# Optimization experiments

Measured on AMD Instinct MI355X. Metric: run time of the kernel, lower is better.

The kernel has to match this reference:

```python
import jax, jax.numpy as jnp
import numpy as np

B, T, F, H, E = 512, 512, 32, 128, 64


def _uniform(key, shape, fan):
    bound = 1.0 / np.sqrt(fan)
    return jax.random.uniform(key, shape, jnp.float32, -bound, bound)


def setup_inputs() -> dict:
    key = jax.random.key(0)
    ks = jax.random.split(key, 9)
    return {
        "x": jax.random.normal(ks[0], (B, T, F), jnp.float32),
        # layer 1: n_features -> hidden_dim (PyTorch gate order i,f,g,o)
        "W_ih1": _uniform(ks[1], (4 * H, F), H),
        "W_hh1": _uniform(ks[2], (4 * H, H), H),
        "b_ih1": _uniform(ks[3], (4 * H,), H),
        "b_hh1": _uniform(ks[4], (4 * H,), H),
        # layer 2: hidden_dim -> embedding_dim
        "W_ih2": _uniform(ks[5], (4 * E, H), E),
        "W_hh2": _uniform(ks[6], (4 * E, E), E),
        "b_ih2": _uniform(ks[7], (4 * E,), E),
        "b_hh2": _uniform(ks[8], (4 * E,), E),
    }


def _lstm(x_seq, W_ih, W_hh, b_ih, b_hh):
    """batch_first LSTM, zero init state. Returns (all_h [B,T,H], last_h [B,H])."""
    b, t, _ = x_seq.shape
    h_dim = W_hh.shape[1]
    # precompute input contributions for the whole sequence: [B,T,4H]
    xg = jnp.einsum('bti,gi->btg', x_seq, W_ih) + b_ih + b_hh

    def step(carry, xt):
        h, c = carry
        gates = xt + h @ W_hh.T  # [B,4H]
        i, f, g, o = jnp.split(gates, 4, axis=-1)
        i = jax.nn.sigmoid(i)
        f = jax.nn.sigmoid(f)
        g = jnp.tanh(g)
        o = jax.nn.sigmoid(o)
        c = f * c + i * g
        h = o * jnp.tanh(c)
        return (h, c), h

    h0 = jnp.zeros((b, h_dim), x_seq.dtype)
    (hT, _), hs = jax.lax.scan(step, (h0, h0), jnp.swapaxes(xg, 0, 1))
    return jnp.swapaxes(hs, 0, 1), hT


def reference(x, W_ih1, W_hh1, b_ih1, b_hh1, W_ih2, W_hh2, b_ih2, b_hh2):
    x = x.reshape((-1, T, F))
    seq1, _ = _lstm(x, W_ih1, W_hh1, b_ih1, b_hh1)       # [B,T,H]
    _, hT = _lstm(seq1, W_ih2, W_hh2, b_ih2, b_hh2)       # [B,E]
    return hT
```

## Files before the change

kernel.cpp:

```cpp
#include <hip/hip_runtime.h>

typedef __attribute__((ext_vector_type(8))) _Float16 halfx8;
typedef __attribute__((ext_vector_type(4))) float f32x4;

#define MFMA16H(a, b, c) __builtin_amdgcn_mfma_f32_16x16x32_f16(a, b, c, 0, 0, 0)

#define T_SEQ 512
#define F_IN 32
#define H1 128
#define E2 64
#define ROWS 4

__device__ __forceinline__ ushort f2h(float f) {
    _Float16 h = (_Float16)f;
    return __builtin_bit_cast(ushort, h);
}
__device__ __forceinline__ float fast_sigmoid(float x) {
    float e = __expf(-x);
    return __builtin_amdgcn_rcpf(1.0f + e);
}
__device__ __forceinline__ float fast_tanh(float x) {
    float e = __expf(-2.0f * x);
    return 2.0f * __builtin_amdgcn_rcpf(1.0f + e) - 1.0f;
}
__device__ __forceinline__ halfx8 load_w8h(const float* p) {
    halfx8 r;
#pragma unroll
    for (int j = 0; j < 8; ++j) r[j] = (_Float16)p[j];
    return r;
}

__global__ __launch_bounds__(512, 1) void lstm_fused(
    const float* __restrict__ x,
    const float* __restrict__ Wih1,
    const float* __restrict__ Whh1,
    const float* __restrict__ bih1,
    const float* __restrict__ bhh1,
    const float* __restrict__ Wih2,
    const float* __restrict__ Whh2,
    const float* __restrict__ bih2,
    const float* __restrict__ bhh2,
    float* __restrict__ out)
{
    __shared__ __align__(16) ushort xs [16][ROWS][80];
    __shared__ __align__(16) ushort h1s[2][ROWS][144];
    __shared__ __align__(16) ushort h2s[2][ROWS][80];

    const int tid  = threadIdx.x;
    const int wave = tid >> 6;
    const int lane = tid & 63;
    const int l15  = lane & 15;
    const int quad = lane >> 4;
    const int arow = l15 >> 2;
    const int r0   = blockIdx.x * ROWS;
    const bool isL1 = (wave < 4);
    const int w    = wave & 3;

    halfx8 wf[40];
    float  bias[8];

    if (isL1) {
#pragma unroll
        for (int g = 0; g < 4; ++g)
#pragma unroll
            for (int uo = 0; uo < 2; ++uo) {
                const int tau = g * 2 + uo;
                const int n = g * 128 + w * 32 + uo * 16 + l15;
#pragma unroll
                for (int kt = 0; kt < 4; ++kt)
                    wf[tau * 4 + kt] = load_w8h(Whh1 + n * H1 + kt * 32 + quad * 8);
                wf[32 + tau] = load_w8h(Wih1 + n * F_IN + quad * 8);
                bias[tau] = bih1[n] + bhh1[n];
            }
    } else {
#pragma unroll
        for (int g = 0; g < 4; ++g) {
            const int n = g * 64 + w * 16 + l15;
#pragma unroll
            for (int kt = 0; kt < 4; ++kt)
                wf[g * 4 + kt] = load_w8h(Wih2 + n * H1 + kt * 32 + quad * 8);
#pragma unroll
            for (int kc = 0; kc < 2; ++kc)
                wf[16 + g * 2 + kc] = load_w8h(Whh2 + n * E2 + kc * 32 + quad * 8);
            bias[g] = bih2[n] + bhh2[n];
        }
    }

    for (int i = tid; i < 2 * ROWS * 144; i += 512) ((ushort*)h1s)[i] = 0;
    for (int i = tid; i < 2 * ROWS * 80;  i += 512) ((ushort*)h2s)[i] = 0;

    float cst[2] = {0.0f, 0.0f};

    const int xrow = w;
    const int xcol = lane;
    const bool stager = (!isL1) && (lane < 32);
    const float* xptr = x + ((size_t)(r0 + xrow) * T_SEQ) * F_IN + xcol;
    float xr8[8];
#pragma unroll
    for (int j = 0; j < 8; ++j) xr8[j] = 0.0f;
    if (stager) {
        float t0[8];
#pragma unroll
        for (int j = 0; j < 8; ++j) t0[j] = xptr[(size_t)j * F_IN];
#pragma unroll
        for (int j = 0; j < 8; ++j) xs[j][xrow][xcol] = f2h(t0[j]);
#pragma unroll
        for (int j = 0; j < 8; ++j) xr8[j] = xptr[(size_t)(8 + j) * F_IN];
    }
    __syncthreads();

    f32x4 acc[8];

#pragma unroll 1
    for (int tt = 0; tt <= T_SEQ; ++tt) {
        const int p  = tt & 1;
        const int pn = p ^ 1;

        if (isL1) {
            if (tt < T_SEQ) {
#pragma unroll
                for (int tau = 0; tau < 8; ++tau)
                    acc[tau] = (f32x4){bias[tau], bias[tau], bias[tau], bias[tau]};
                __builtin_amdgcn_s_setprio(1);
                {
                    const halfx8 ax = *(const halfx8*)&xs[tt & 15][arow][quad * 8];
#pragma unroll
                    for (int tau = 0; tau < 8; ++tau)
                        acc[tau] = MFMA16H(ax, wf[32 + tau], acc[tau]);
                }
#pragma unroll
                for (int kt = 0; kt < 4; ++kt) {
                    const halfx8 a = *(const halfx8*)&h1s[p][arow][kt * 32 + quad * 8];
#pragma unroll
                    for (int tau = 0; tau < 8; ++tau)
                        acc[tau] = MFMA16H(a, wf[tau * 4 + kt], acc[tau]);
                }
                __builtin_amdgcn_s_setprio(0);
#pragma unroll
                for (int uo = 0; uo < 2; ++uo) {
                    const int u = w * 32 + uo * 16 + l15;
                    const float iv = fast_sigmoid(acc[0 + uo][0]);
                    const float fv = fast_sigmoid(acc[2 + uo][0]);
                    const float gv = fast_tanh   (acc[4 + uo][0]);
                    const float ov = fast_sigmoid(acc[6 + uo][0]);
                    const float cn = fv * cst[uo] + iv * gv;
                    cst[uo] = cn;
                    const float h = ov * fast_tanh(cn);
                    h1s[pn][quad][u] = f2h(h);
                }
            }
        } else {
            if (tt >= 1) {
#pragma unroll
                for (int g = 0; g < 4; ++g)
                    acc[g] = (f32x4){bias[g], bias[g], bias[g], bias[g]};
                __builtin_amdgcn_s_setprio(1);
#pragma unroll
                for (int kt = 0; kt < 4; ++kt) {
                    const halfx8 a = *(const halfx8*)&h1s[p][arow][kt * 32 + quad * 8];
#pragma unroll
                    for (int g = 0; g < 4; ++g)
                        acc[g] = MFMA16H(a, wf[g * 4 + kt], acc[g]);
                }
#pragma unroll
                for (int kc = 0; kc < 2; ++kc) {
                    const halfx8 a = *(const halfx8*)&h2s[p][arow][kc * 32 + quad * 8];
#pragma unroll
                    for (int g = 0; g < 4; ++g)
                        acc[g] = MFMA16H(a, wf[16 + g * 2 + kc], acc[g]);
                }
                __builtin_amdgcn_s_setprio(0);
                const int u = w * 16 + l15;
                const float iv = fast_sigmoid(acc[0][0]);
                const float fv = fast_sigmoid(acc[1][0]);
                const float gv = fast_tanh   (acc[2][0]);
                const float ov = fast_sigmoid(acc[3][0]);
                const float cn = fv * cst[0] + iv * gv;
                cst[0] = cn;
                const float h = ov * fast_tanh(cn);
                if (tt == T_SEQ) {
                    out[(size_t)(r0 + quad) * E2 + u] = h;
                } else {
                    h2s[pn][quad][u] = f2h(h);
                }
            }
            if (stager && (tt & 7) == 0) {
#pragma unroll
                for (int j = 0; j < 8; ++j) {
                    const int t = tt + 8 + j;
                    if (t < T_SEQ) xs[t & 15][xrow][xcol] = f2h(xr8[j]);
                }
#pragma unroll
                for (int j = 0; j < 8; ++j) {
                    const int t = tt + 16 + j;
                    if (t < T_SEQ) xr8[j] = xptr[(size_t)t * F_IN];
                }
            }
        }
        __syncthreads();
    }
}

extern "C" void kernel_launch(void* const* d_in, const int* in_sizes, int n_in,
                              void* d_out, int out_size, void* d_ws, size_t ws_size,
                              hipStream_t stream) {
    lstm_fused<<<128, 512, 0, stream>>>(
        (const float*)d_in[0], (const float*)d_in[1], (const float*)d_in[2],
        (const float*)d_in[3], (const float*)d_in[4], (const float*)d_in[5],
        (const float*)d_in[6], (const float*)d_in[7], (const float*)d_in[8],
        (float*)d_out);
}
```

Measured before the change: 475.4 us.

## Offload layer-1 input projection to layer-2 waves, batched four timesteps ahead

The layer-1 input projection (x·W_ih1 + bias) moves off the critical layer-1 recurrence. The layer-2 waves now compute it every 4 steps, one MFMA per gate tile covering 4 timesteps × 4 rows, and write it into an 8-slot LDS ring. The layer-1 waves then run only the recurrent h·W_hh1 MFMAs and add the precomputed gate inputs. The aim is to shorten the serial per-step chain on the layer-1 waves. The cost is extra LDS traffic, extra register pressure on the layer-2 waves, and relying on the ring's slot timing staying correct.

```diff
diff --git a/kernel.cpp b/kernel.cpp
--- a/kernel.cpp
+++ b/kernel.cpp
@@ -42,9 +42,11 @@
     const float* __restrict__ bhh2,
     float* __restrict__ out)
 {
-    __shared__ __align__(16) ushort xs [16][ROWS][80];
+    __shared__ __align__(16) ushort xa [4][16][40];
+    __shared__ __align__(16) float  xgl[8 * 2088];
     __shared__ __align__(16) ushort h1s[2][ROWS][144];
     __shared__ __align__(16) ushort h2s[2][ROWS][80];
+#define XGI(s, r, u) ((s) * 2088 + (r) * 520 + (u) * 4)
 
     const int tid  = threadIdx.x;
     const int wave = tid >> 6;
@@ -56,8 +58,8 @@
     const bool isL1 = (wave < 4);
     const int w    = wave & 3;
 
-    halfx8 wf[40];
-    float  bias[8];
+    halfx8 wf[32];
+    float  bias2[4], bx[8];
 
     if (isL1) {
 #pragma unroll
@@ -69,21 +71,28 @@
 #pragma unroll
                 for (int kt = 0; kt < 4; ++kt)
                     wf[tau * 4 + kt] = load_w8h(Whh1 + n * H1 + kt * 32 + quad * 8);
-                wf[32 + tau] = load_w8h(Wih1 + n * F_IN + quad * 8);
-                bias[tau] = bih1[n] + bhh1[n];
             }
     } else {
 #pragma unroll
         for (int g = 0; g < 4; ++g) {
-            const int n = g * 64 + w * 16 + l15;
+            const int n2 = g * 64 + w * 16 + l15;
 #pragma unroll
             for (int kt = 0; kt < 4; ++kt)
-                wf[g * 4 + kt] = load_w8h(Wih2 + n * H1 + kt * 32 + quad * 8);
+                wf[g * 4 + kt] = load_w8h(Wih2 + n2 * H1 + kt * 32 + quad * 8);
 #pragma unroll
             for (int kc = 0; kc < 2; ++kc)
-                wf[16 + g * 2 + kc] = load_w8h(Whh2 + n * E2 + kc * 32 + quad * 8);
-            bias[g] = bih2[n] + bhh2[n];
+                wf[16 + g * 2 + kc] = load_w8h(Whh2 + n2 * E2 + kc * 32 + quad * 8);
+            bias2[g] = bih2[n2] + bhh2[n2];
         }
+#pragma unroll
+        for (int g = 0; g < 4; ++g)
+#pragma unroll
+            for (int uo = 0; uo < 2; ++uo) {
+                const int tau = g * 2 + uo;
+                const int n = g * 128 + w * 32 + uo * 16 + l15;
+                wf[24 + tau] = load_w8h(Wih1 + n * F_IN + quad * 8);
+                bx[tau] = bih1[n] + bhh1[n];
+            }
     }
 
     for (int i = tid; i < 2 * ROWS * 144; i += 512) ((ushort*)h1s)[i] = 0;
@@ -91,10 +100,8 @@
 
     float cst[2] = {0.0f, 0.0f};
 
-    const int xrow = w;
-    const int xcol = lane;
     const bool stager = (!isL1) && (lane < 32);
-    const float* xptr = x + ((size_t)(r0 + xrow) * T_SEQ) * F_IN + xcol;
+    const float* xptr = x + ((size_t)(r0 + w) * T_SEQ) * F_IN + lane;
     float xr8[8];
 #pragma unroll
     for (int j = 0; j < 8; ++j) xr8[j] = 0.0f;
@@ -103,13 +110,27 @@
 #pragma unroll
         for (int j = 0; j < 8; ++j) t0[j] = xptr[(size_t)j * F_IN];
 #pragma unroll
-        for (int j = 0; j < 8; ++j) xs[j][xrow][xcol] = f2h(t0[j]);
+        for (int j = 0; j < 8; ++j)
+            xa[(j >> 2) & 3][(j & 3) * 4 + w][lane] = f2h(t0[j]);
 #pragma unroll
         for (int j = 0; j < 8; ++j) xr8[j] = xptr[(size_t)(8 + j) * F_IN];
     }
     __syncthreads();
 
-    f32x4 acc[8];
+    if (!isL1) {
+        const halfx8 af = *(const halfx8*)&xa[0][l15][quad * 8];
+#pragma unroll
+        for (int nt = 0; nt < 8; ++nt) {
+            const float b = bx[nt];
+            const f32x4 cinit = {b, b, b, b};
+            const f32x4 d = MFMA16H(af, wf[24 + nt], cinit);
+            const int uu = w * 32 + (nt & 1) * 16 + l15;
+#pragma unroll
+            for (int j = 0; j < 4; ++j)
+                xgl[XGI(quad, j, uu) + (nt >> 1)] = d[j];
+        }
+    }
+    __syncthreads();
 
 #pragma unroll 1
     for (int tt = 0; tt <= T_SEQ; ++tt) {
@@ -118,31 +139,31 @@
 
         if (isL1) {
             if (tt < T_SEQ) {
+                const f32x4 xg0 = *(const f32x4*)&xgl[XGI(tt & 7, quad, w * 32 + l15)];
+                const f32x4 xg1 = *(const f32x4*)&xgl[XGI(tt & 7, quad, w * 32 + 16 + l15)];
+                halfx8 hf[4];
+#pragma unroll
+                for (int kt = 0; kt < 4; ++kt)
+                    hf[kt] = *(const halfx8*)&h1s[p][arow][kt * 32 + quad * 8];
+                f32x4 acc[8];
 #pragma unroll
                 for (int tau = 0; tau < 8; ++tau)
-                    acc[tau] = (f32x4){bias[tau], bias[tau], bias[tau], bias[tau]};
+                    acc[tau] = (f32x4){0.0f, 0.0f, 0.0f, 0.0f};
                 __builtin_amdgcn_s_setprio(1);
-                {
-                    const halfx8 ax = *(const halfx8*)&xs[tt & 15][arow][quad * 8];
+#pragma unroll
+                for (int kt = 0; kt < 4; ++kt)
 #pragma unroll
                     for (int tau = 0; tau < 8; ++tau)
-                        acc[tau] = MFMA16H(ax, wf[32 + tau], acc[tau]);
-                }
-#pragma unroll
-                for (int kt = 0; kt < 4; ++kt) {
-                    const halfx8 a = *(const halfx8*)&h1s[p][arow][kt * 32 + quad * 8];
-#pragma unroll
-                    for (int tau = 0; tau < 8; ++tau)
-                        acc[tau] = MFMA16H(a, wf[tau * 4 + kt], acc[tau]);
-                }
+                        acc[tau] = MFMA16H(hf[kt], wf[tau * 4 + kt], acc[tau]);
                 __builtin_amdgcn_s_setprio(0);
 #pragma unroll
                 for (int uo = 0; uo < 2; ++uo) {
+                    const f32x4 xgv = uo ? xg1 : xg0;
                     const int u = w * 32 + uo * 16 + l15;
-                    const float iv = fast_sigmoid(acc[0 + uo][0]);
-                    const float fv = fast_sigmoid(acc[2 + uo][0]);
-                    const float gv = fast_tanh   (acc[4 + uo][0]);
-                    const float ov = fast_sigmoid(acc[6 + uo][0]);
+                    const float iv = fast_sigmoid(acc[0 + uo][0] + xgv[0]);
+                    const float fv = fast_sigmoid(acc[2 + uo][0] + xgv[1]);
+                    const float gv = fast_tanh   (acc[4 + uo][0] + xgv[2]);
+                    const float ov = fast_sigmoid(acc[6 + uo][0] + xgv[3]);
                     const float cn = fv * cst[uo] + iv * gv;
                     cst[uo] = cn;
                     const float h = ov * fast_tanh(cn);
@@ -151,30 +172,31 @@
             }
         } else {
             if (tt >= 1) {
+                f32x4 acc2[4];
 #pragma unroll
                 for (int g = 0; g < 4; ++g)
-                    acc[g] = (f32x4){bias[g], bias[g], bias[g], bias[g]};
+                    acc2[g] = (f32x4){bias2[g], bias2[g], bias2[g], bias2[g]};
                 __builtin_amdgcn_s_setprio(1);
 #pragma unroll
                 for (int kt = 0; kt < 4; ++kt) {
                     const halfx8 a = *(const halfx8*)&h1s[p][arow][kt * 32 + quad * 8];
 #pragma unroll
                     for (int g = 0; g < 4; ++g)
-                        acc[g] = MFMA16H(a, wf[g * 4 + kt], acc[g]);
+                        acc2[g] = MFMA16H(a, wf[g * 4 + kt], acc2[g]);
                 }
 #pragma unroll
                 for (int kc = 0; kc < 2; ++kc) {
                     const halfx8 a = *(const halfx8*)&h2s[p][arow][kc * 32 + quad * 8];
 #pragma unroll
                     for (int g = 0; g < 4; ++g)
-                        acc[g] = MFMA16H(a, wf[16 + g * 2 + kc], acc[g]);
+                        acc2[g] = MFMA16H(a, wf[16 + g * 2 + kc], acc2[g]);
                 }
                 __builtin_amdgcn_s_setprio(0);
                 const int u = w * 16 + l15;
-                const float iv = fast_sigmoid(acc[0][0]);
-                const float fv = fast_sigmoid(acc[1][0]);
-                const float gv = fast_tanh   (acc[2][0]);
-                const float ov = fast_sigmoid(acc[3][0]);
+                const float iv = fast_sigmoid(acc2[0][0]);
+                const float fv = fast_sigmoid(acc2[1][0]);
+                const float gv = fast_tanh   (acc2[2][0]);
+                const float ov = fast_sigmoid(acc2[3][0]);
                 const float cn = fv * cst[0] + iv * gv;
                 cst[0] = cn;
                 const float h = ov * fast_tanh(cn);
@@ -184,11 +206,29 @@
                     h2s[pn][quad][u] = f2h(h);
                 }
             }
+            if ((tt & 3) == 0) {
+                const int tb = (tt >> 2) + 1;
+                if (tb < (T_SEQ >> 2)) {
+                    const halfx8 af = *(const halfx8*)&xa[tb & 3][l15][quad * 8];
+#pragma unroll
+                    for (int nt = 0; nt < 8; ++nt) {
+                        const float b = bx[nt];
+                        const f32x4 cinit = {b, b, b, b};
+                        const f32x4 d = MFMA16H(af, wf[24 + nt], cinit);
+                        const int uu = w * 32 + (nt & 1) * 16 + l15;
+                        const int slot = (tb * 4 + quad) & 7;
+#pragma unroll
+                        for (int j = 0; j < 4; ++j)
+                            xgl[XGI(slot, j, uu) + (nt >> 1)] = d[j];
+                    }
+                }
+            }
             if (stager && (tt & 7) == 0) {
 #pragma unroll
                 for (int j = 0; j < 8; ++j) {
                     const int t = tt + 8 + j;
-                    if (t < T_SEQ) xs[t & 15][xrow][xcol] = f2h(xr8[j]);
+                    if (t < T_SEQ)
+                        xa[(t >> 2) & 3][(t & 3) * 4 + w][lane] = f2h(xr8[j]);
                 }
 #pragma unroll
                 for (int j = 0; j < 8; ++j) {
@@ -199,6 +239,7 @@
         }
         __syncthreads();
     }
+#undef XGI
 }
 
 extern "C" void kernel_launch(void* const* d_in, const int* in_sizes, int n_in,
```

Result: slower. 516.1 us (+8.6%).

## Split layer-1 LSTM work across eight waves with 768-thread blocks

Applied to the files above, without the earlier changes.

Layer 1 now runs on 8 waves instead of 4, each owning 16 hidden units (4 gate tiles) instead of 32, which halves the serial MFMA chain per wave on the critical recurrent step. Blocks grow to 768 threads, and layer-2 waves become waves 8-11. The h1 LDS fragments are also loaded up front, before the MFMA chain starts. The cost is more waves per CU taking part in each per-step barrier, plus more threads contending for the single CU's issue slots.

```diff
diff --git a/kernel.cpp b/kernel.cpp
--- a/kernel.cpp
+++ b/kernel.cpp
@@ -30,7 +30,7 @@
     return r;
 }
 
-__global__ __launch_bounds__(512, 1) void lstm_fused(
+__global__ __launch_bounds__(768, 1) void lstm_fused(
     const float* __restrict__ x,
     const float* __restrict__ Wih1,
     const float* __restrict__ Whh1,
@@ -53,29 +53,26 @@
     const int quad = lane >> 4;
     const int arow = l15 >> 2;
     const int r0   = blockIdx.x * ROWS;
-    const bool isL1 = (wave < 4);
-    const int w    = wave & 3;
-
-    halfx8 wf[40];
-    float  bias[8];
+    const bool isL1 = (wave < 8);
+
+    halfx8 wf[24];
+    float  bias[4];
 
     if (isL1) {
 #pragma unroll
-        for (int g = 0; g < 4; ++g)
-#pragma unroll
-            for (int uo = 0; uo < 2; ++uo) {
-                const int tau = g * 2 + uo;
-                const int n = g * 128 + w * 32 + uo * 16 + l15;
-#pragma unroll
-                for (int kt = 0; kt < 4; ++kt)
-                    wf[tau * 4 + kt] = load_w8h(Whh1 + n * H1 + kt * 32 + quad * 8);
-                wf[32 + tau] = load_w8h(Wih1 + n * F_IN + quad * 8);
-                bias[tau] = bih1[n] + bhh1[n];
-            }
+        for (int g = 0; g < 4; ++g) {
+            const int n = g * 128 + wave * 16 + l15;
+#pragma unroll
+            for (int kt = 0; kt < 4; ++kt)
+                wf[g * 4 + kt] = load_w8h(Whh1 + n * H1 + kt * 32 + quad * 8);
+            wf[16 + g] = load_w8h(Wih1 + n * F_IN + quad * 8);
+            bias[g] = bih1[n] + bhh1[n];
+        }
     } else {
+        const int w2 = wave - 8;
 #pragma unroll
         for (int g = 0; g < 4; ++g) {
-            const int n = g * 64 + w * 16 + l15;
+            const int n = g * 64 + w2 * 16 + l15;
 #pragma unroll
             for (int kt = 0; kt < 4; ++kt)
                 wf[g * 4 + kt] = load_w8h(Wih2 + n * H1 + kt * 32 + quad * 8);
@@ -86,15 +83,14 @@
         }
     }
 
-    for (int i = tid; i < 2 * ROWS * 144; i += 512) ((ushort*)h1s)[i] = 0;
-    for (int i = tid; i < 2 * ROWS * 80;  i += 512) ((ushort*)h2s)[i] = 0;
-
-    float cst[2] = {0.0f, 0.0f};
-
-    const int xrow = w;
-    const int xcol = lane;
+    for (int i = tid; i < 2 * ROWS * 144; i += 768) ((ushort*)h1s)[i] = 0;
+    for (int i = tid; i < 2 * ROWS * 80;  i += 768) ((ushort*)h2s)[i] = 0;
+
+    float cst = 0.0f;
+
+    const int w2s  = wave & 3;
     const bool stager = (!isL1) && (lane < 32);
-    const float* xptr = x + ((size_t)(r0 + xrow) * T_SEQ) * F_IN + xcol;
+    const float* xptr = x + ((size_t)(r0 + w2s) * T_SEQ) * F_IN + lane;
     float xr8[8];
 #pragma unroll
     for (int j = 0; j < 8; ++j) xr8[j] = 0.0f;
@@ -103,13 +99,11 @@
 #pragma unroll
         for (int j = 0; j < 8; ++j) t0[j] = xptr[(size_t)j * F_IN];
 #pragma unroll
-        for (int j = 0; j < 8; ++j) xs[j][xrow][xcol] = f2h(t0[j]);
+        for (int j = 0; j < 8; ++j) xs[j][w2s][lane] = f2h(t0[j]);
 #pragma unroll
         for (int j = 0; j < 8; ++j) xr8[j] = xptr[(size_t)(8 + j) * F_IN];
     }
     __syncthreads();
-
-    f32x4 acc[8];
 
 #pragma unroll 1
     for (int tt = 0; tt <= T_SEQ; ++tt) {
@@ -118,65 +112,64 @@
 
         if (isL1) {
             if (tt < T_SEQ) {
-#pragma unroll
-                for (int tau = 0; tau < 8; ++tau)
-                    acc[tau] = (f32x4){bias[tau], bias[tau], bias[tau], bias[tau]};
-                __builtin_amdgcn_s_setprio(1);
-                {
-                    const halfx8 ax = *(const halfx8*)&xs[tt & 15][arow][quad * 8];
-#pragma unroll
-                    for (int tau = 0; tau < 8; ++tau)
-                        acc[tau] = MFMA16H(ax, wf[32 + tau], acc[tau]);
-                }
-#pragma unroll
-                for (int kt = 0; kt < 4; ++kt) {
-                    const halfx8 a = *(const halfx8*)&h1s[p][arow][kt * 32 + quad * 8];
-#pragma unroll
-                    for (int tau = 0; tau < 8; ++tau)
-                        acc[tau] = MFMA16H(a, wf[tau * 4 + kt], acc[tau]);
-                }
-                __builtin_amdgcn_s_setprio(0);
-#pragma unroll
-                for (int uo = 0; uo < 2; ++uo) {
-                    const int u = w * 32 + uo * 16 + l15;
-                    const float iv = fast_sigmoid(acc[0 + uo][0]);
-                    const float fv = fast_sigmoid(acc[2 + uo][0]);
-                    const float gv = fast_tanh   (acc[4 + uo][0]);
-                    const float ov = fast_sigmoid(acc[6 + uo][0]);
-                    const float cn = fv * cst[uo] + iv * gv;
-                    cst[uo] = cn;
-                    const float h = ov * fast_tanh(cn);
-                    h1s[pn][quad][u] = f2h(h);
-                }
-            }
-        } else {
-            if (tt >= 1) {
+                f32x4 acc[4];
 #pragma unroll
                 for (int g = 0; g < 4; ++g)
                     acc[g] = (f32x4){bias[g], bias[g], bias[g], bias[g]};
+                const halfx8 ax = *(const halfx8*)&xs[tt & 15][arow][quad * 8];
+                halfx8 hf[4];
+#pragma unroll
+                for (int kt = 0; kt < 4; ++kt)
+                    hf[kt] = *(const halfx8*)&h1s[p][arow][kt * 32 + quad * 8];
                 __builtin_amdgcn_s_setprio(1);
 #pragma unroll
-                for (int kt = 0; kt < 4; ++kt) {
-                    const halfx8 a = *(const halfx8*)&h1s[p][arow][kt * 32 + quad * 8];
+                for (int g = 0; g < 4; ++g)
+                    acc[g] = MFMA16H(ax, wf[16 + g], acc[g]);
+#pragma unroll
+                for (int kt = 0; kt < 4; ++kt)
 #pragma unroll
                     for (int g = 0; g < 4; ++g)
-                        acc[g] = MFMA16H(a, wf[g * 4 + kt], acc[g]);
-                }
-#pragma unroll
-                for (int kc = 0; kc < 2; ++kc) {
-                    const halfx8 a = *(const halfx8*)&h2s[p][arow][kc * 32 + quad * 8];
-#pragma unroll
-                    for (int g = 0; g < 4; ++g)
-                        acc[g] = MFMA16H(a, wf[16 + g * 2 + kc], acc[g]);
-                }
+                        acc[g] = MFMA16H(hf[kt], wf[g * 4 + kt], acc[g]);
                 __builtin_amdgcn_s_setprio(0);
-                const int u = w * 16 + l15;
+                const int u = wave * 16 + l15;
                 const float iv = fast_sigmoid(acc[0][0]);
                 const float fv = fast_sigmoid(acc[1][0]);
                 const float gv = fast_tanh   (acc[2][0]);
                 const float ov = fast_sigmoid(acc[3][0]);
-                const float cn = fv * cst[0] + iv * gv;
-                cst[0] = cn;
+                const float cn = fv * cst + iv * gv;
+                cst = cn;
+                const float h = ov * fast_tanh(cn);
+                h1s[pn][quad][u] = f2h(h);
+            }
+        } else {
+            if (tt >= 1) {
+                f32x4 acc2[4];
+#pragma unroll
+                for (int g = 0; g < 4; ++g)
+                    acc2[g] = (f32x4){bias[g], bias[g], bias[g], bias[g]};
+                __builtin_amdgcn_s_setprio(1);
+#pragma unroll
+                for (int kt = 0; kt < 4; ++kt) {
+                    const halfx8 a = *(const halfx8*)&h1s[p][arow][kt * 32 + quad * 8];
+#pragma unroll
+                    for (int g = 0; g < 4; ++g)
+                        acc2[g] = MFMA16H(a, wf[g * 4 + kt], acc2[g]);
+                }
+#pragma unroll
+                for (int kc = 0; kc < 2; ++kc) {
+                    const halfx8 a = *(const halfx8*)&h2s[p][arow][kc * 32 + quad * 8];
+#pragma unroll
+                    for (int g = 0; g < 4; ++g)
+                        acc2[g] = MFMA16H(a, wf[16 + g * 2 + kc], acc2[g]);
+                }
+                __builtin_amdgcn_s_setprio(0);
+                const int u = (wave - 8) * 16 + l15;
+                const float iv = fast_sigmoid(acc2[0][0]);
+                const float fv = fast_sigmoid(acc2[1][0]);
+                const float gv = fast_tanh   (acc2[2][0]);
+                const float ov = fast_sigmoid(acc2[3][0]);
+                const float cn = fv * cst + iv * gv;
+                cst = cn;
                 const float h = ov * fast_tanh(cn);
                 if (tt == T_SEQ) {
                     out[(size_t)(r0 + quad) * E2 + u] = h;
@@ -188,7 +181,7 @@
 #pragma unroll
                 for (int j = 0; j < 8; ++j) {
                     const int t = tt + 8 + j;
-                    if (t < T_SEQ) xs[t & 15][xrow][xcol] = f2h(xr8[j]);
+                    if (t < T_SEQ) xs[t & 15][w2s][lane] = f2h(xr8[j]);
                 }
 #pragma unroll
                 for (int j = 0; j < 8; ++j) {
@@ -204,7 +197,7 @@
 extern "C" void kernel_launch(void* const* d_in, const int* in_sizes, int n_in,
                               void* d_out, int out_size, void* d_ws, size_t ws_size,
                               hipStream_t stream) {
-    lstm_fused<<<128, 512, 0, stream>>>(
+    lstm_fused<<<128, 768, 0, stream>>>(
         (const float*)d_in[0], (const float*)d_in[1], (const float*)d_in[2],
         (const float*)d_in[3], (const float*)d_in[4], (const float*)d_in[5],
         (const float*)d_in[6], (const float*)d_in[7], (const float*)d_in[8],
```

Result: no change. 483.3 us (+1.7%).
